# Performance work log

Hardware: AMD Instinct MI355X
Metric: run time of the kernel (lower is better)

The kernel has to match this reference:

```python
import jax, jax.numpy as jnp
import numpy as np

B, P, O, C = 64, 8732, 32, 81
IMG = 224.0
THRESH = 0.5
NEG_POS = 3.0
ALPHA = 1.0


def cxcy_to_xy(b):
    return jnp.concatenate([b[..., :2] - b[..., 2:] / 2, b[..., :2] + b[..., 2:] / 2], -1)


def xy_to_cxcy(b):
    return jnp.concatenate([(b[..., :2] + b[..., 2:]) / 2, b[..., 2:] - b[..., :2]], -1)


def coco_to_xy(b):  # [x, y, w, h] -> [xmin, ymin, xmax, ymax]
    return jnp.concatenate([b[..., :2], b[..., :2] + b[..., 2:]], -1)


def cxcy_to_gcxgcy(cxcy, priors):  # SSD offset encoding, variances 10 / 5
    g_cxcy = (cxcy[..., :2] - priors[..., :2]) / (priors[..., 2:] / 10.0)
    g_wh = jnp.log(cxcy[..., 2:] / priors[..., 2:]) * 5.0
    return jnp.concatenate([g_cxcy, g_wh], -1)


def pairwise_iou(a, b):  # a: [O,4] xy, b: [P,4] xy -> [O,P]
    lt = jnp.maximum(a[:, None, :2], b[None, :, :2])
    rb = jnp.minimum(a[:, None, 2:], b[None, :, 2:])
    wh = jnp.clip(rb - lt, 0.0)
    inter = wh[..., 0] * wh[..., 1]
    area_a = (a[:, 2] - a[:, 0]) * (a[:, 3] - a[:, 1])
    area_b = (b[:, 2] - b[:, 0]) * (b[:, 3] - b[:, 1])
    return inter / (area_a[:, None] + area_b[None, :] - inter)


def setup_inputs() -> dict:
    key = jax.random.key(0)
    k1, k2, k3, k4, k5, k6, k7 = jax.random.split(key, 7)
    pred_locs = jax.random.normal(k1, (B, P, 4), dtype=jnp.float32)
    pred_scores = jax.random.normal(k2, (B, P, C), dtype=jnp.float32)
    # COCO-format gt boxes [x, y, w, h] in pixel coords, guaranteed inside image
    xy = jax.random.uniform(k3, (B, O, 2), minval=0.0, maxval=IMG * 0.55)
    wh = jax.random.uniform(k4, (B, O, 2), minval=8.0, maxval=IMG * 0.4)
    gt_boxes = jnp.concatenate([xy, wh], -1)
    gt_labels = jax.random.randint(k5, (B, O), 1, C)  # foreground labels 1..C-1
    p_cxcy = jax.random.uniform(k6, (P, 2), minval=0.05, maxval=0.95)
    p_wh = jax.random.uniform(k7, (P, 2), minval=0.05, maxval=0.5)
    priors_cxcy = jnp.concatenate([p_cxcy, p_wh], -1)
    return {"pred_locs": pred_locs, "pred_scores": pred_scores,
            "gt_boxes": gt_boxes, "gt_labels": gt_labels,
            "priors_cxcy": priors_cxcy}


def reference(pred_locs, pred_scores, gt_boxes, gt_labels, priors_cxcy):
    priors_xy = cxcy_to_xy(priors_cxcy)

    def match(boxes_coco, labels):  # one image: [O,4] coco, [O] int
        boxes_xy = coco_to_xy(boxes_coco) / IMG  # normalize to [0,1]
        ov = pairwise_iou(boxes_xy, priors_xy)  # [O, P]
        overlap_for_prior = ov.max(axis=0)       # [P]
        object_for_prior = ov.argmax(axis=0)     # [P]
        prior_for_object = ov.argmax(axis=1)     # [O]
        # force each object to claim its best prior
        object_for_prior = object_for_prior.at[prior_for_object].set(jnp.arange(O))
        overlap_for_prior = overlap_for_prior.at[prior_for_object].set(1.0)
        label_for_prior = labels[object_for_prior]
        label_for_prior = jnp.where(overlap_for_prior < THRESH, 0, label_for_prior)
        true_locs = cxcy_to_gcxgcy(xy_to_cxcy(boxes_xy[object_for_prior]), priors_cxcy)
        return true_locs, label_for_prior

    true_locs, true_classes = jax.vmap(match)(gt_boxes, gt_labels)  # [B,P,4], [B,P]

    positive = true_classes != 0          # [B, P]
    n_pos = positive.sum(axis=1)          # [B]
    n_pos_cl = jnp.maximum(n_pos, 1).astype(jnp.float32)
    n_hard_neg = NEG_POS * n_pos_cl

    # SmoothL1 (beta=1), mean over positive prior coords
    diff = jnp.abs(pred_locs - true_locs)
    sl1 = jnp.where(diff < 1.0, 0.5 * diff * diff, diff - 0.5)  # [B,P,4]
    total_pos = n_pos.sum()
    loc_loss = jnp.where(
        total_pos > 0,
        jnp.where(positive[..., None], sl1, 0.0).sum()
        / jnp.maximum(total_pos * 4, 1).astype(jnp.float32),
        0.0,
    )

    # per-prior cross entropy
    logp = jax.nn.log_softmax(pred_scores, axis=-1)
    ce = -jnp.take_along_axis(logp, true_classes[..., None], axis=-1)[..., 0]  # [B,P]

    conf_pos_sum = jnp.where(positive, ce, 0.0).sum()
    ce_neg = jnp.where(positive, 0.0, ce)
    ce_neg_sorted = -jnp.sort(-ce_neg, axis=1)  # descending per image
    ranks = jnp.arange(P)[None, :]
    hard = ranks < n_hard_neg[:, None]
    conf_hard_neg_sum = jnp.where(hard, ce_neg_sorted, 0.0).sum()

    conf_loss = (conf_hard_neg_sum + conf_pos_sum) / n_pos_cl.sum()
    return conf_loss + ALPHA * loc_loss
```

## Files before the change

### kernel.cpp

```cpp
#include <hip/hip_runtime.h>
#include <cstdint>
#include <cstddef>

#define BB 64
#define PP 8732
#define OO 32
#define CC 81
#define NQ 4
#define QP 2183
#define NR4 128
#define NB4 69

__global__ __launch_bounds__(1024) void k_prep(
    const float* __restrict__ gt_boxes,
    const float4* __restrict__ priors,
    unsigned long long* __restrict__ part,
    int* __restrict__ done)
{
    int q = blockIdx.x, b = blockIdx.y, t = threadIdx.x;
    if (q == 0 && b == 0 && t == 0) *done = 0;
    int o = t >> 5, s = t & 31;
    __shared__ float4 s_pr[1024];
    const float* g = gt_boxes + ((size_t)b * OO + o) * 4;
    float x1 = g[0] / 224.0f, y1 = g[1] / 224.0f;
    float x2 = (g[0] + g[2]) / 224.0f, y2 = (g[1] + g[3]) / 224.0f;
    float area = (x2 - x1) * (y2 - y1);
    float best = -1.0f; int bp = 0;
    int p0 = q * QP;
    for (int base = 0; base < QP; base += 1024) {
        int idx = base + t;
        if (idx < QP) s_pr[t] = priors[p0 + idx];
        __syncthreads();
        int lim = QP - base; if (lim > 1024) lim = 1024;
        for (int j = s; j < lim; j += 128) {
            float iou4[4]; int jj4[4];
            #pragma unroll
            for (int u = 0; u < 4; ++u) {
                int jj = j + 32 * u;
                jj4[u] = jj;
                if (jj < lim) {
                    float4 pr = s_pr[jj];
                    float px1 = pr.x - pr.z * 0.5f, py1 = pr.y - pr.w * 0.5f;
                    float px2 = pr.x + pr.z * 0.5f, py2 = pr.y + pr.w * 0.5f;
                    float parea = (px2 - px1) * (py2 - py1);
                    float lx = fmaxf(x1, px1), ly = fmaxf(y1, py1);
                    float rx = fminf(x2, px2), ry = fminf(y2, py2);
                    float w = fmaxf(rx - lx, 0.0f), h = fmaxf(ry - ly, 0.0f);
                    float inter = w * h;
                    iou4[u] = inter / (area + parea - inter);
                } else iou4[u] = -2.0f;
            }
            #pragma unroll
            for (int u = 0; u < 4; ++u)
                if (iou4[u] > best) { best = iou4[u]; bp = p0 + base + jj4[u]; }
        }
        __syncthreads();
    }
    unsigned long long v = ((unsigned long long)__float_as_uint(best) << 32)
                         | (unsigned long long)(0xFFFFFFFFu - (unsigned)bp);
    #pragma unroll
    for (int sh = 16; sh >= 1; sh >>= 1) {
        unsigned long long u = __shfl_xor(v, sh, 32);
        if (u > v) v = u;
    }
    if (s == 0) part[((size_t)b * NQ + q) * OO + o] = v;
}

__global__ __launch_bounds__(128) void k_ce(
    const float* __restrict__ scores,
    const float4* __restrict__ pred_locs,
    const float* __restrict__ gt_boxes,
    const int* __restrict__ gt_labels,
    const float4* __restrict__ priors,
    const unsigned long long* __restrict__ part,
    float* __restrict__ ceneg,
    float* __restrict__ pp_posce, float* __restrict__ pp_sl1,
    int* __restrict__ pp_np)
{
    int b = blockIdx.y, tid = threadIdx.x;
    int row0 = blockIdx.x * NR4;
    int nrows = PP - row0; if (nrows > NR4) nrows = NR4;

    __shared__ float sv[NR4 * CC];
    __shared__ float bx1[OO], by1[OO], bx2[OO], by2[OO], bar[OO];
    __shared__ int s_lab[OO];
    __shared__ int s_pfo[OO];
    __shared__ int s_force[NR4];
    __shared__ float s_posce, s_sl1;
    __shared__ int s_np;

    if (tid == 0) { s_posce = 0.f; s_sl1 = 0.f; s_np = 0; }
    if (tid < OO) {
        const float* g = gt_boxes + ((size_t)b * OO + tid) * 4;
        float x1 = g[0] / 224.0f, y1 = g[1] / 224.0f;
        float x2 = (g[0] + g[2]) / 224.0f, y2 = (g[1] + g[3]) / 224.0f;
        bx1[tid] = x1; by1[tid] = y1; bx2[tid] = x2; by2[tid] = y2;
        bar[tid] = (x2 - x1) * (y2 - y1);
        s_lab[tid] = gt_labels[b * OO + tid];
        const unsigned long long* pb = part + (size_t)b * NQ * OO + tid;
        unsigned long long m = pb[0];
        #pragma unroll
        for (int qq = 1; qq < NQ; ++qq) {
            unsigned long long v = pb[qq * OO];
            if (v > m) m = v;
        }
        s_pfo[tid] = (int)(0xFFFFFFFFu - (unsigned)(m & 0xFFFFFFFFull));
    }
    s_force[tid] = -1;
    __syncthreads();
    if (tid == 0) {
        #pragma unroll
        for (int o = 0; o < OO; ++o) {
            int rp = s_pfo[o] - row0;
            if (rp >= 0 && rp < nrows) s_force[rp] = o;
        }
    }
    {
        const float4* src4 = (const float4*)(scores + ((size_t)b * PP + row0) * CC);
        float4* dst = (float4*)sv;
        int nvec = nrows * CC / 4;
        for (int base = 0; base < nvec; base += 512) {
            int i0 = base + tid, i1 = i0 + 128, i2 = i0 + 256, i3 = i0 + 384;
            bool v0 = i0 < nvec, v1 = i1 < nvec, v2 = i2 < nvec, v3 = i3 < nvec;
            float4 t0, t1, t2, t3;
            if (v0) t0 = src4[i0];
            if (v1) t1 = src4[i1];
            if (v2) t2 = src4[i2];
            if (v3) t3 = src4[i3];
            if (v0) dst[i0] = t0;
            if (v1) dst[i1] = t1;
            if (v2) dst[i2] = t2;
            if (v3) dst[i3] = t3;
        }
    }
    __syncthreads();

    if (tid < nrows) {
        int p = row0 + tid;
        float4 pq = priors[p];
        float px1 = pq.x - pq.z * 0.5f, py1 = pq.y - pq.w * 0.5f;
        float px2 = pq.x + pq.z * 0.5f, py2 = pq.y + pq.w * 0.5f;
        float parea = (px2 - px1) * (py2 - py1);
        float bi = -1.0f; int bo = 0;
        #pragma unroll
        for (int o = 0; o < OO; ++o) {
            float lx = fmaxf(bx1[o], px1), ly = fmaxf(by1[o], py1);
            float rx = fminf(bx2[o], px2), ry = fminf(by2[o], py2);
            float w = fmaxf(rx - lx, 0.0f), h = fmaxf(ry - ly, 0.0f);
            float inter = w * h;
            float iou = inter / (bar[o] + parea - inter);
            if (iou > bi) { bi = iou; bo = o; }
        }
        int fo = s_force[tid];
        int lab, ob;
        if (fo >= 0) { ob = fo; lab = s_lab[fo]; }
        else         { ob = bo; lab = (bi < 0.5f) ? 0 : s_lab[bo]; }
        const float* row = sv + tid * CC;
        float se0 = 0.f, se1 = 0.f, se2 = 0.f, se3 = 0.f;
        #pragma unroll
        for (int c = 0; c < 80; c += 4) {
            se0 += __expf(row[c]);
            se1 += __expf(row[c + 1]);
            se2 += __expf(row[c + 2]);
            se3 += __expf(row[c + 3]);
        }
        float se = (se0 + se1) + (se2 + se3) + __expf(row[80]);
        float xl = row[lab];
        float ce = fmaxf(__logf(se) - xl, 0.0f);
        float cn = ce;
        if (lab != 0) {
            cn = 0.f;
            float4 pl = pred_locs[(size_t)b * PP + p];
            float x1 = bx1[ob], y1 = by1[ob], x2 = bx2[ob], y2 = by2[ob];
            float cx = (x1 + x2) * 0.5f, cy = (y1 + y2) * 0.5f;
            float w = x2 - x1, h = y2 - y1;
            float tx = (cx - pq.x) / (pq.z / 10.0f);
            float ty = (cy - pq.y) / (pq.w / 10.0f);
            float tw = __logf(w / pq.z) * 5.0f;
            float th = __logf(h / pq.w) * 5.0f;
            float d0 = fabsf(pl.x - tx), d1 = fabsf(pl.y - ty);
            float d2 = fabsf(pl.z - tw), d3 = fabsf(pl.w - th);
            float sl = (d0 < 1.f ? 0.5f * d0 * d0 : d0 - 0.5f)
                     + (d1 < 1.f ? 0.5f * d1 * d1 : d1 - 0.5f)
                     + (d2 < 1.f ? 0.5f * d2 * d2 : d2 - 0.5f)
                     + (d3 < 1.f ? 0.5f * d3 * d3 : d3 - 0.5f);
            atomicAdd(&s_posce, ce);
            atomicAdd(&s_sl1, sl);
            atomicAdd(&s_np, 1);
        }
        ceneg[(size_t)b * PP + p] = cn;
    }
    __syncthreads();
    if (tid == 0) {
        int slot = b * NB4 + blockIdx.x;
        pp_posce[slot] = s_posce;
        pp_sl1[slot]   = s_sl1;
        pp_np[slot]    = s_np;
    }
}

__global__ __launch_bounds__(512) void k_topk(
    const float* __restrict__ ceneg,
    const float* __restrict__ pp_posce, const float* __restrict__ pp_sl1,
    const int* __restrict__ pp_np,
    float* __restrict__ hard, float* __restrict__ posce_b,
    float* __restrict__ sl1_b, int* __restrict__ n_pos,
    int* __restrict__ done, float* __restrict__ out)
{
    int b = blockIdx.x, tid = threadIdx.x;
    __shared__ float4 sv4[PP / 4];
    __shared__ int hist[8][256];
    __shared__ int hsum[256];
    __shared__ int s_i[8];
    __shared__ float s_f[8], s_f2[8];
    __shared__ int s_bcast;
    __shared__ unsigned s_sel;
    __shared__ int s_krem;
    __shared__ int s_last;
    float pc = 0.f, sl = 0.f; int np = 0;
    for (int i = tid; i < NB4; i += 512) {
        pc += pp_posce[b * NB4 + i];
        sl += pp_sl1[b * NB4 + i];
        np += pp_np[b * NB4 + i];
    }
    #pragma unroll
    for (int s = 32; s >= 1; s >>= 1) {
        pc += __shfl_xor(pc, s, 64);
        sl += __shfl_xor(sl, s, 64);
        np += __shfl_xor(np, s, 64);
    }
    int wid = tid >> 6;
    if ((tid & 63) == 0) { s_i[wid] = np; s_f[wid] = pc; s_f2[wid] = sl; }
    const float4* src = (const float4*)(ceneg + (size_t)b * PP);
    for (int i = tid; i < PP / 4; i += 512) sv4[i] = src[i];
    __syncthreads();
    if (tid == 0) {
        int n = 0; float fp = 0.f, fs = 0.f;
        #pragma unroll
        for (int k = 0; k < 8; ++k) { n += s_i[k]; fp += s_f[k]; fs += s_f2[k]; }
        n_pos[b] = n; posce_b[b] = fp; sl1_b[b] = fs;
        s_bcast = n;
        int K0 = 3 * (n > 1 ? n : 1);
        if (K0 > PP) K0 = PP;
        s_sel = 0u; s_krem = K0;
    }
    __syncthreads();
    np = s_bcast;
    int K = 3 * (np > 1 ? np : 1);
    if (K > PP) K = PP;
    #pragma unroll
    for (int s = 24; s >= 0; s -= 8) {
        for (int i = tid; i < 8 * 256; i += 512) ((int*)hist)[i] = 0;
        __syncthreads();
        unsigned pref = s_sel; int krem = s_krem;
        int hs = s + 8;
        unsigned prefhi = (hs >= 32) ? 0u : (pref >> (hs & 31));
        for (int i = tid; i < PP / 4; i += 512) {
            float4 q = sv4[i];
            float vals[4] = {q.x, q.y, q.z, q.w};
            #pragma unroll
            for (int c4 = 0; c4 < 4; ++c4) {
                unsigned bts = __float_as_uint(vals[c4]);
                bool ok = (hs >= 32) || ((bts >> (hs & 31)) == prefhi);
                if (ok) atomicAdd(&hist[wid][(bts >> s) & 255], 1);
            }
        }
        __syncthreads();
        if (tid < 256) {
            int t = 0;
            #pragma unroll
            for (int k = 0; k < 8; ++k) t += hist[k][tid];
            hsum[tid] = t;
        }
        __syncthreads();
        if (tid < 64) {
            int ln = tid;
            int cum = 0;
            for (int c = 3; c >= 0; --c) {
                int h = hsum[c * 64 + ln];
                int suff = h;
                #pragma unroll
                for (int off = 1; off < 64; off <<= 1) {
                    int t = __shfl_down(suff, off);
                    if (ln + off < 64) suff += t;
                }
                int ctot = __shfl(suff, 0);
                if (cum + ctot >= krem) {
                    unsigned long long m = __ballot(cum + suff >= krem);
                    int l = 63 - __builtin_clzll(m);
                    int suffl = __shfl(suff, l);
                    int hl = __shfl(h, l);
                    if (ln == 0) {
                        s_sel = pref | ((unsigned)(c * 64 + l) << s);
                        s_krem = krem - (cum + suffl - hl);
                    }
                    break;
                }
                cum += ctot;
            }
        }
        __syncthreads();
    }
    float vk = __uint_as_float(s_sel);
    float sm = 0.f; int cg = 0;
    for (int i = tid; i < PP / 4; i += 512) {
        float4 q = sv4[i];
        if (q.x > vk) { sm += q.x; cg++; }
        if (q.y > vk) { sm += q.y; cg++; }
        if (q.z > vk) { sm += q.z; cg++; }
        if (q.w > vk) { sm += q.w; cg++; }
    }
    #pragma unroll
    for (int s = 32; s >= 1; s >>= 1) {
        sm += __shfl_xor(sm, s, 64);
        cg += __shfl_xor(cg, s, 64);
    }
    if ((tid & 63) == 0) { s_f[wid] = sm; s_i[wid] = cg; }
    __syncthreads();
    if (tid == 0) {
        float S = 0.f; int CG = 0;
        #pragma unroll
        for (int k = 0; k < 8; ++k) { S += s_f[k]; CG += s_i[k]; }
        hard[b] = S + (float)(K - CG) * vk;
    }
    __threadfence();
    if (tid == 0) s_last = (atomicAdd(done, 1) == BB - 1) ? 1 : 0;
    __syncthreads();
    if (s_last) {
        __threadfence();
        if (tid < 64) {
            int t = tid;
            int np2 = n_pos[t];
            float h2 = hard[t], pc2 = posce_b[t], sl2 = sl1_b[t];
            float cl = (float)(np2 > 1 ? np2 : 1);
            int tp = np2; float hs2 = h2; float cls = cl;
            #pragma unroll
            for (int sft = 32; sft >= 1; sft >>= 1) {
                tp  += __shfl_xor(tp, sft, 64);
                hs2 += __shfl_xor(hs2, sft, 64);
                cls += __shfl_xor(cls, sft, 64);
                pc2 += __shfl_xor(pc2, sft, 64);
                sl2 += __shfl_xor(sl2, sft, 64);
            }
            if (t == 0) {
                float conf = (hs2 + pc2) / cls;
                float loc = 0.f;
                if (tp > 0) {
                    int den = tp * 4; if (den < 1) den = 1;
                    loc = sl2 / (float)den;
                }
                out[0] = conf + loc;
            }
        }
    }
}

extern "C" void kernel_launch(void* const* d_in, const int* in_sizes, int n_in,
                              void* d_out, int out_size, void* d_ws, size_t ws_size,
                              hipStream_t stream)
{
    const float* pred_locs   = (const float*)d_in[0];
    const float* pred_scores = (const float*)d_in[1];
    const float* gt_boxes    = (const float*)d_in[2];
    const int*   gt_labels   = (const int*)d_in[3];
    const float* priors      = (const float*)d_in[4];

    char* ws = (char*)d_ws;
    const size_t npf = (size_t)BB * PP;
    size_t off = 0;
    float* ceneg = (float*)(ws + off); off += 4 * npf;
    unsigned long long* part = (unsigned long long*)(ws + off); off += 8 * (size_t)BB * NQ * OO;
    float* pp_posce = (float*)(ws + off); off += 4 * (size_t)BB * NB4;
    float* pp_sl1   = (float*)(ws + off); off += 4 * (size_t)BB * NB4;
    int*   pp_np    = (int*)  (ws + off); off += 4 * (size_t)BB * NB4;
    float* posce_b  = (float*)(ws + off); off += 4 * BB;
    float* sl1_b    = (float*)(ws + off); off += 4 * BB;
    int*   n_pos    = (int*)  (ws + off); off += 4 * BB;
    float* hard     = (float*)(ws + off); off += 4 * BB;
    int*   done     = (int*)  (ws + off); off += 4;

    dim3 gP(NQ, BB);
    k_prep<<<gP, 1024, 0, stream>>>(gt_boxes, (const float4*)priors, part, done);

    dim3 gB(NB4, BB);
    k_ce<<<gB, 128, 0, stream>>>(pred_scores, (const float4*)pred_locs, gt_boxes, gt_labels,
                                 (const float4*)priors, part, ceneg,
                                 pp_posce, pp_sl1, pp_np);

    k_topk<<<BB, 512, 0, stream>>>(ceneg, pp_posce, pp_sl1, pp_np,
                                   hard, posce_b, sl1_b, n_pos, done, (float*)d_out);
}
```

Before: 333.4 us.

## Compute cross entropy directly from global memory with 16-lane groups per row

The k_ce kernel no longer stages the whole score tile in shared memory. Each row's logsumexp is now computed by a 16-thread group that reads the scores straight from global memory and reduces with shuffles, which cuts the large LDS footprint and should raise occupancy. Blocks grow to 256 rows and 256 threads. The forced-match lookup moves into the IoU loop as a per-object comparison. The trade-off is strided, less coalesced global reads and an extra shared-memory round trip for labels and CE values.

```diff
diff --git a/kernel.cpp b/kernel.cpp
--- a/kernel.cpp
+++ b/kernel.cpp
@@ -8,8 +8,8 @@
 #define CC 81
 #define NQ 4
 #define QP 2183
-#define NR4 128
-#define NB4 69
+#define NR5 256
+#define NB5 35
 
 __global__ __launch_bounds__(1024) void k_prep(
     const float* __restrict__ gt_boxes,
@@ -66,7 +66,7 @@
     if (s == 0) part[((size_t)b * NQ + q) * OO + o] = v;
 }
 
-__global__ __launch_bounds__(128) void k_ce(
+__global__ __launch_bounds__(256) void k_ce(
     const float* __restrict__ scores,
     const float4* __restrict__ pred_locs,
     const float* __restrict__ gt_boxes,
@@ -78,14 +78,14 @@
     int* __restrict__ pp_np)
 {
     int b = blockIdx.y, tid = threadIdx.x;
-    int row0 = blockIdx.x * NR4;
-    int nrows = PP - row0; if (nrows > NR4) nrows = NR4;
-
-    __shared__ float sv[NR4 * CC];
+    int row0 = blockIdx.x * NR5;
+    int nrows = PP - row0; if (nrows > NR5) nrows = NR5;
+
     __shared__ float bx1[OO], by1[OO], bx2[OO], by2[OO], bar[OO];
     __shared__ int s_lab[OO];
     __shared__ int s_pfo[OO];
-    __shared__ int s_force[NR4];
+    __shared__ int s_ol[NR5];
+    __shared__ float s_cn[NR5];
     __shared__ float s_posce, s_sl1;
     __shared__ int s_np;
 
@@ -106,33 +106,6 @@
         }
         s_pfo[tid] = (int)(0xFFFFFFFFu - (unsigned)(m & 0xFFFFFFFFull));
     }
-    s_force[tid] = -1;
-    __syncthreads();
-    if (tid == 0) {
-        #pragma unroll
-        for (int o = 0; o < OO; ++o) {
-            int rp = s_pfo[o] - row0;
-            if (rp >= 0 && rp < nrows) s_force[rp] = o;
-        }
-    }
-    {
-        const float4* src4 = (const float4*)(scores + ((size_t)b * PP + row0) * CC);
-        float4* dst = (float4*)sv;
-        int nvec = nrows * CC / 4;
-        for (int base = 0; base < nvec; base += 512) {
-            int i0 = base + tid, i1 = i0 + 128, i2 = i0 + 256, i3 = i0 + 384;
-            bool v0 = i0 < nvec, v1 = i1 < nvec, v2 = i2 < nvec, v3 = i3 < nvec;
-            float4 t0, t1, t2, t3;
-            if (v0) t0 = src4[i0];
-            if (v1) t1 = src4[i1];
-            if (v2) t2 = src4[i2];
-            if (v3) t3 = src4[i3];
-            if (v0) dst[i0] = t0;
-            if (v1) dst[i1] = t1;
-            if (v2) dst[i2] = t2;
-            if (v3) dst[i3] = t3;
-        }
-    }
     __syncthreads();
 
     if (tid < nrows) {
@@ -141,8 +114,8 @@
         float px1 = pq.x - pq.z * 0.5f, py1 = pq.y - pq.w * 0.5f;
         float px2 = pq.x + pq.z * 0.5f, py2 = pq.y + pq.w * 0.5f;
         float parea = (px2 - px1) * (py2 - py1);
-        float bi = -1.0f; int bo = 0;
-        #pragma unroll
+        float bi = -1.0f; int bo = 0; int fo = -1;
+        #pragma unroll 8
         for (int o = 0; o < OO; ++o) {
             float lx = fmaxf(bx1[o], px1), ly = fmaxf(by1[o], py1);
             float rx = fminf(bx2[o], px2), ry = fminf(by2[o], py2);
@@ -150,26 +123,13 @@
             float inter = w * h;
             float iou = inter / (bar[o] + parea - inter);
             if (iou > bi) { bi = iou; bo = o; }
-        }
-        int fo = s_force[tid];
+            if (s_pfo[o] == p) fo = o;
+        }
         int lab, ob;
         if (fo >= 0) { ob = fo; lab = s_lab[fo]; }
         else         { ob = bo; lab = (bi < 0.5f) ? 0 : s_lab[bo]; }
-        const float* row = sv + tid * CC;
-        float se0 = 0.f, se1 = 0.f, se2 = 0.f, se3 = 0.f;
-        #pragma unroll
-        for (int c = 0; c < 80; c += 4) {
-            se0 += __expf(row[c]);
-            se1 += __expf(row[c + 1]);
-            se2 += __expf(row[c + 2]);
-            se3 += __expf(row[c + 3]);
-        }
-        float se = (se0 + se1) + (se2 + se3) + __expf(row[80]);
-        float xl = row[lab];
-        float ce = fmaxf(__logf(se) - xl, 0.0f);
-        float cn = ce;
+        s_ol[tid] = lab;
         if (lab != 0) {
-            cn = 0.f;
             float4 pl = pred_locs[(size_t)b * PP + p];
             float x1 = bx1[ob], y1 = by1[ob], x2 = bx2[ob], y2 = by2[ob];
             float cx = (x1 + x2) * 0.5f, cy = (y1 + y2) * 0.5f;
@@ -184,15 +144,47 @@
                      + (d1 < 1.f ? 0.5f * d1 * d1 : d1 - 0.5f)
                      + (d2 < 1.f ? 0.5f * d2 * d2 : d2 - 0.5f)
                      + (d3 < 1.f ? 0.5f * d3 * d3 : d3 - 0.5f);
-            atomicAdd(&s_posce, ce);
             atomicAdd(&s_sl1, sl);
             atomicAdd(&s_np, 1);
         }
-        ceneg[(size_t)b * PP + p] = cn;
-    }
-    __syncthreads();
+    }
+    __syncthreads();
+
+    {
+        int g = tid >> 4, lane = tid & 15;
+        #pragma unroll 4
+        for (int j = 0; j < 16; ++j) {
+            int r = g + 16 * j;
+            if (r < nrows) {
+                int lab = s_ol[r];
+                const float* row = scores + ((size_t)b * PP + row0 + r) * CC;
+                float se = 0.f, xl = 0.f;
+                #pragma unroll
+                for (int k = 0; k < 6; ++k) {
+                    int c = lane + 16 * k;
+                    if (c < CC) {
+                        float v = row[c];
+                        se += __expf(v);
+                        if (c == lab) xl = v;
+                    }
+                }
+                #pragma unroll
+                for (int s = 8; s >= 1; s >>= 1) {
+                    se += __shfl_xor(se, s, 16);
+                    xl += __shfl_xor(xl, s, 16);
+                }
+                if (lane == 0) {
+                    float ce = fmaxf(__logf(se) - xl, 0.0f);
+                    if (lab != 0) { atomicAdd(&s_posce, ce); s_cn[r] = 0.f; }
+                    else s_cn[r] = ce;
+                }
+            }
+        }
+    }
+    __syncthreads();
+    if (tid < nrows) ceneg[(size_t)b * PP + row0 + tid] = s_cn[tid];
     if (tid == 0) {
-        int slot = b * NB4 + blockIdx.x;
+        int slot = b * NB5 + blockIdx.x;
         pp_posce[slot] = s_posce;
         pp_sl1[slot]   = s_sl1;
         pp_np[slot]    = s_np;
@@ -218,10 +210,10 @@
     __shared__ int s_krem;
     __shared__ int s_last;
     float pc = 0.f, sl = 0.f; int np = 0;
-    for (int i = tid; i < NB4; i += 512) {
-        pc += pp_posce[b * NB4 + i];
-        sl += pp_sl1[b * NB4 + i];
-        np += pp_np[b * NB4 + i];
+    for (int i = tid; i < NB5; i += 512) {
+        pc += pp_posce[b * NB5 + i];
+        sl += pp_sl1[b * NB5 + i];
+        np += pp_np[b * NB5 + i];
     }
     #pragma unroll
     for (int s = 32; s >= 1; s >>= 1) {
@@ -370,9 +362,9 @@
     size_t off = 0;
     float* ceneg = (float*)(ws + off); off += 4 * npf;
     unsigned long long* part = (unsigned long long*)(ws + off); off += 8 * (size_t)BB * NQ * OO;
-    float* pp_posce = (float*)(ws + off); off += 4 * (size_t)BB * NB4;
-    float* pp_sl1   = (float*)(ws + off); off += 4 * (size_t)BB * NB4;
-    int*   pp_np    = (int*)  (ws + off); off += 4 * (size_t)BB * NB4;
+    float* pp_posce = (float*)(ws + off); off += 4 * (size_t)BB * NB5;
+    float* pp_sl1   = (float*)(ws + off); off += 4 * (size_t)BB * NB5;
+    int*   pp_np    = (int*)  (ws + off); off += 4 * (size_t)BB * NB5;
     float* posce_b  = (float*)(ws + off); off += 4 * BB;
     float* sl1_b    = (float*)(ws + off); off += 4 * BB;
     int*   n_pos    = (int*)  (ws + off); off += 4 * BB;
@@ -382,8 +374,8 @@
     dim3 gP(NQ, BB);
     k_prep<<<gP, 1024, 0, stream>>>(gt_boxes, (const float4*)priors, part, done);
 
-    dim3 gB(NB4, BB);
-    k_ce<<<gB, 128, 0, stream>>>(pred_scores, (const float4*)pred_locs, gt_boxes, gt_labels,
+    dim3 gB(NB5, BB);
+    k_ce<<<gB, 256, 0, stream>>>(pred_scores, (const float4*)pred_locs, gt_boxes, gt_labels,
                                  (const float4*)priors, part, ceneg,
                                  pp_posce, pp_sl1, pp_np);
 
```

New measurement: 325.3 us. 2.4% less time.
